# Kernel optimization log

Measured on AMD Instinct MI355X. Metric: run time of the kernel, lower is better.

The kernel has to match this reference:

```python
import jax, jax.numpy as jnp
import numpy as np

IN_CH = 256
OUT_CH = 256
STATE = 384
OUT_SEQ = 32
B_SZ = 8
SEQ = 512


def setup_inputs() -> dict:
    key = jax.random.key(0)
    ks = jax.random.split(key, 8)
    rmin, rmax, max_phase = 0.0, 1.0, 6.283
    u1 = jax.random.uniform(ks[0], (STATE,))
    u2 = jax.random.uniform(ks[1], (STATE,))
    # standard LRU stable-ring initialization
    nu_log = jnp.log(-0.5 * jnp.log(u1 * (rmax + rmin) * (rmax - rmin) + rmin ** 2))
    theta_log = jnp.log(max_phase * u2)
    lam_mod = jnp.exp(-jnp.exp(nu_log))
    gamma_log = jnp.log(jnp.sqrt(1.0 - lam_mod ** 2))
    B_re = jax.random.normal(ks[2], (STATE, IN_CH)) / np.sqrt(2 * IN_CH)
    B_im = jax.random.normal(ks[3], (STATE, IN_CH)) / np.sqrt(2 * IN_CH)
    C_re = jax.random.normal(ks[4], (OUT_CH, STATE)) / np.sqrt(STATE)
    C_im = jax.random.normal(ks[5], (OUT_CH, STATE)) / np.sqrt(STATE)
    D = jax.random.normal(ks[6], (OUT_CH, IN_CH)) / np.sqrt(IN_CH)
    x = jax.random.normal(ks[7], (B_SZ, SEQ, IN_CH))
    return dict(x=x, nu_log=nu_log, theta_log=theta_log, gamma_log=gamma_log,
                B_re=B_re, B_im=B_im, C_re=C_re, C_im=C_im, D=D)


def _lru(x, h_re, h_im, nu_log, theta_log, gamma_log, B_re, B_im, C_re, C_im, D):
    """One LRU pass over a full sequence. x: [B,S,C]. h_*: [B,N] initial complex state.
    Diagonal complex recurrence h_t = Lambda*h_{t-1} + gamma*(B x_t); y_t = Re(C h_t) + D x_t."""
    lam_mod = jnp.exp(-jnp.exp(nu_log))              # |Lambda| in (0,1)
    lre = lam_mod * jnp.cos(jnp.exp(theta_log))      # [N]
    lim = lam_mod * jnp.sin(jnp.exp(theta_log))
    gamma = jnp.exp(gamma_log)
    # input projection for whole sequence (complex, split into re/im)
    u_re = gamma * jnp.einsum('bsc,nc->bsn', x, B_re)  # [B,S,N]
    u_im = gamma * jnp.einsum('bsc,nc->bsn', x, B_im)

    def step(h, u):
        hre, him = h
        ur, ui = u
        nre = lre * hre - lim * him + ur
        nim = lre * him + lim * hre + ui
        return (nre, nim), (nre, nim)

    (h_re, h_im), (hs_re, hs_im) = jax.lax.scan(
        step, (h_re, h_im),
        (jnp.swapaxes(u_re, 0, 1), jnp.swapaxes(u_im, 0, 1)))  # scan over S
    hs_re = jnp.swapaxes(hs_re, 0, 1)  # [B,S,N]
    hs_im = jnp.swapaxes(hs_im, 0, 1)
    y = (jnp.einsum('bsn,on->bso', hs_re, C_re)
         - jnp.einsum('bsn,on->bso', hs_im, C_im)
         + jnp.einsum('bsc,oc->bso', x, D))
    return y, h_re, h_im


def reference(x, nu_log, theta_log, gamma_log, B_re, B_im, C_re, C_im, D):
    bsz = x.shape[0]
    h_re = jnp.zeros((bsz, STATE), x.dtype)   # state=None on first call -> zeros
    h_im = jnp.zeros((bsz, STATE), x.dtype)
    outs = []
    for _ in range(OUT_SEQ):
        x, h_re, h_im = _lru(x, h_re, h_im, nu_log, theta_log, gamma_log,
                             B_re, B_im, C_re, C_im, D)
        outs.append(x[:, -1:])
    return jnp.concatenate(outs, axis=-2)  # [B, OUT_SEQ, OUT_CH]
```

## Files before the change

### kernel.cpp

```cpp
#include <hip/hip_runtime.h>
#include <hip/hip_bf16.h>
#include <math.h>

typedef unsigned short u16;
typedef __attribute__((ext_vector_type(8))) short bf16x8;
typedef __attribute__((ext_vector_type(4))) float f32x4;
typedef __attribute__((ext_vector_type(16))) float f32x16;

#define IN_CH   256
#define STATE   384
#define OUT_SEQ 32
#define B_SZ    8
#define SEQ     512
#define M_ROWS  4096
#define NJ      768

#define PS_WB  (NJ*IN_CH)
#define PS_WC  (IN_CH*NJ)
#define PS_WD  (IN_CH*IN_CH)
#define PS_Z   ((size_t)M_ROWS*NJ)
#define PS_X   ((size_t)M_ROWS*IN_CH)

static constexpr size_t B_U   = 0;
static constexpr size_t B_Z   = B_U  + 8*(size_t)M_ROWS*IN_CH*4;
static constexpr size_t B_XA  = B_Z  + 3*(size_t)M_ROWS*NJ*2;
static constexpr size_t B_XB  = B_XA + 3*(size_t)M_ROWS*IN_CH*2;
static constexpr size_t B_WB  = B_XB + 3*(size_t)M_ROWS*IN_CH*2;
static constexpr size_t B_WC  = B_WB + 3*(size_t)PS_WB*2;
static constexpr size_t B_WD  = B_WC + 3*(size_t)PS_WC*2;
static constexpr size_t B_LAM = B_WD + 3*(size_t)PS_WD*2;
static constexpr size_t B_HC  = B_LAM + 2*768*4;

__device__ __forceinline__ u16 f2b(float v) {
    __hip_bfloat16 h = __float2bfloat16(v);
    return *(u16*)&h;
}
__device__ __forceinline__ float b2f(u16 u) {
    __hip_bfloat16 h = *(__hip_bfloat16*)&u;
    return __bfloat162float(h);
}
__device__ __forceinline__ void split3(float v, u16& a, u16& b, u16& c) {
    a = f2b(v);  float r1 = v  - b2f(a);
    b = f2b(r1); float r2 = r1 - b2f(b);
    c = f2b(r2);
}

__device__ __forceinline__ size_t a_idx(int row, int k, int NKC) {
    return ((size_t)(((row >> 5)*NKC + (k >> 5))*2 + ((k >> 4) & 1))*2 + ((k >> 3) & 1))*256
           + (size_t)(row & 31)*8 + (k & 7);
}

__device__ __forceinline__ void frag_decode(int r, int& t32, int& h, int& hi5,
                                            int& lo5, int& e) {
    t32 = r >> 10; int r2 = r & 1023;
    h = r2 >> 9;   int r3 = r2 & 511;
    hi5 = r3 >> 8; int r4 = r3 & 255;
    lo5 = r4 >> 3; e = r4 & 7;
}

__global__ void prep_lam_hc(const float* __restrict__ nu_log,
                            const float* __restrict__ th_log,
                            float* __restrict__ lam, float* __restrict__ lam16,
                            float* __restrict__ hc0) {
    int n = threadIdx.x;
    if (n < STATE) {
        float lm = expf(-expf(nu_log[n]));
        float th = expf(th_log[n]);
        float ar = lm * cosf(th), ai = lm * sinf(th);
        lam[2*n] = ar; lam[2*n+1] = ai;
        float pr = ar, pi = ai;
#pragma unroll
        for (int i = 0; i < 4; ++i) {
            float nr = pr*pr - pi*pi, ni = 2.f*pr*pi;
            pr = nr; pi = ni;
        }
        lam16[2*n] = pr; lam16[2*n+1] = pi;
    }
    for (int i = threadIdx.x; i < B_SZ*NJ; i += blockDim.x) hc0[i] = 0.f;
}

__global__ void prep_big(const float* __restrict__ B_re, const float* __restrict__ B_im,
                         const float* __restrict__ gamma_log,
                         const float* __restrict__ C_re, const float* __restrict__ C_im,
                         const float* __restrict__ D, const float* __restrict__ x,
                         u16* __restrict__ W, u16* __restrict__ WC, u16* __restrict__ WD,
                         u16* __restrict__ X1, u16* __restrict__ X2, u16* __restrict__ X3) {
    int idx = blockIdx.x*blockDim.x + threadIdx.x;
    if (idx < PS_WB) {
        int c32 = idx >> 13, r = idx & 8191;
        int t32,h,hi5,lo5,e; frag_decode(r, t32,h,hi5,lo5,e);
        int j = c32*32 + lo5;
        int k = t32*32 + (2*h + hi5)*8 + e;
        int n = j >> 1;
        float g = expf(gamma_log[n]);
        float v = g * ((j & 1) ? B_im[n*IN_CH + k] : B_re[n*IN_CH + k]);
        u16 a,b,cc; split3(v,a,b,cc);
        W[idx] = a; W[idx + PS_WB] = b; W[idx + 2*PS_WB] = cc;
        return;
    }
    idx -= PS_WB;
    if (idx < PS_WC) {
        int c32 = idx / 24576, r = idx % 24576;
        int t32,h,hi5,lo5,e; frag_decode(r, t32,h,hi5,lo5,e);
        int o = c32*32 + lo5;
        int j = t32*32 + (2*h + hi5)*8 + e;
        int n = j >> 1;
        float v = (j & 1) ? -C_im[o*STATE + n] : C_re[o*STATE + n];
        u16 a,b,c; split3(v,a,b,c);
        WC[idx] = a; WC[idx + PS_WC] = b; WC[idx + 2*PS_WC] = c;
        return;
    }
    idx -= PS_WC;
    if (idx < PS_WD) {
        int c32 = idx >> 13, r = idx & 8191;
        int t32,h,hi5,lo5,e; frag_decode(r, t32,h,hi5,lo5,e);
        int o = c32*32 + lo5;
        int c = t32*32 + (2*h + hi5)*8 + e;
        float v = D[o*IN_CH + c];
        u16 a,b,cc; split3(v,a,b,cc);
        WD[idx] = a; WD[idx + PS_WD] = b; WD[idx + 2*PS_WD] = cc;
        return;
    }
    idx -= PS_WD;
    {
        int row = idx >> 8, k = idx & 255;
        u16 a,b,c; split3(x[idx],a,b,c);
        size_t o = a_idx(row, k, 8);
        X1[o] = a; X2[o] = b; X3[o] = c;
    }
}

__device__ __constant__ const int cPI[6] = {0,0,1,0,1,2};
__device__ __constant__ const int cPJ[6] = {0,1,0,2,1,0};

struct G1P { const u16* A[3]; };

__global__ __launch_bounds__(512, 2)
void front_k(G1P ga, const u16* __restrict__ WBp, const u16* __restrict__ WDp,
             u16* __restrict__ Z1, u16* __restrict__ Z2, u16* __restrict__ Z3,
             float* __restrict__ P,
             const float* __restrict__ lam, const float* __restrict__ lam16,
             const float2* __restrict__ HcIn, float2* __restrict__ HcOut) {
    __shared__ __align__(16) float Ls[512*34];
    __shared__ float2 car[32][16];
    __shared__ float2 hp[32][16];
    const int tid = threadIdx.x, lane = tid & 63, w = tid >> 6;
    const int l15 = lane & 15, q = lane >> 4;
    const int hb = q >> 1, hi5q = q & 1;
    const int hi5 = lane >> 5, lo5 = lane & 31;

    if (blockIdx.x >= 192) {
        const int k0 = blockIdx.x - 192;
        const int mt = (k0 & 7)*8 + (k0 >> 3);
        const int wr = w & 1, wc = w >> 1;
        const int m32 = mt*2 + wr;
        f32x16 acc[2];
#pragma unroll
        for (int cj = 0; cj < 2; ++cj)
#pragma unroll
            for (int i = 0; i < 16; ++i) acc[cj][i] = 0.f;

        bf16x8 av[2][3][2], bv[2][2][3][2];
        auto loadA = [&](int buf, int kc) {
#pragma unroll
            for (int p = 0; p < 3; ++p)
#pragma unroll
                for (int h = 0; h < 2; ++h)
                    av[buf][p][h] = *(const bf16x8*)(ga.A[p]
                        + ((((size_t)(m32*8 + kc)*2 + h)*2 + hi5) << 8) + lo5*8);
        };
        auto loadB = [&](int buf, int kc) {
#pragma unroll
            for (int cj = 0; cj < 2; ++cj)
#pragma unroll
                for (int p = 0; p < 3; ++p)
#pragma unroll
                    for (int h = 0; h < 2; ++h)
                        bv[buf][cj][p][h] = *(const bf16x8*)(WDp + (size_t)p*PS_WD
                            + ((((size_t)((wc*2 + cj)*8 + kc)*2 + h)*2 + hi5) << 8) + lo5*8);
        };
        loadA(0, 0); loadB(0, 0);
        loadA(1, 1); loadB(1, 1);
#pragma unroll
        for (int kc = 0; kc < 8; ++kc) {
            const int cb = kc & 1;
#pragma unroll
            for (int t6 = 0; t6 < 6; ++t6)
#pragma unroll
                for (int cj = 0; cj < 2; ++cj)
#pragma unroll
                    for (int h = 0; h < 2; ++h)
                        acc[cj] = __builtin_amdgcn_mfma_f32_32x32x16_bf16(
                            av[cb][cPI[t6]][h], bv[cb][cj][cPJ[t6]][h], acc[cj], 0, 0, 0);
            if (kc + 2 < 8) { loadA(cb, kc + 2); loadB(cb, kc + 2); }
        }
#pragma unroll
        for (int cj = 0; cj < 2; ++cj)
#pragma unroll
            for (int reg = 0; reg < 16; ++reg) {
                int row = mt*64 + wr*32 + (reg & 3) + 8*(reg >> 2) + 4*hi5;
                int col = wc*64 + cj*32 + lo5;
                P[(size_t)row*IN_CH + col] = acc[cj][reg];
            }
        return;
    }

    const int b = blockIdx.x & 7, jt = blockIdx.x >> 3;

    f32x4 acc[4][2];
#pragma unroll
    for (int i = 0; i < 4; ++i)
#pragma unroll
        for (int n16 = 0; n16 < 2; ++n16) acc[i][n16] = 0.f;

    bf16x8 av[2][4][3], bv[2][2][3];
    auto loadA = [&](int buf, int kc) {
#pragma unroll
        for (int p = 0; p < 3; ++p)
#pragma unroll
            for (int i = 0; i < 4; ++i) {
                int m16 = i*8 + w;
                int row32 = b*16 + (m16 >> 1);
                int rin = ((m16 & 1) << 4) + l15;
                av[buf][i][p] = *(const bf16x8*)(ga.A[p]
                    + ((((size_t)(row32*8 + kc)*2 + hb)*2 + hi5q) << 8) + rin*8);
            }
    };
    auto loadB = [&](int buf, int kc) {
#pragma unroll
        for (int p = 0; p < 3; ++p)
#pragma unroll
            for (int n16 = 0; n16 < 2; ++n16)
                bv[buf][n16][p] = *(const bf16x8*)(WBp + (size_t)p*PS_WB
                    + ((((size_t)(jt*8 + kc)*2 + hb)*2 + hi5q) << 8) + (n16*16 + l15)*8);
    };

    loadA(0, 0); loadB(0, 0);
    loadA(1, 1); loadB(1, 1);
#pragma unroll
    for (int kc = 0; kc < 8; ++kc) {
        const int cb = kc & 1;
#pragma unroll
        for (int t6 = 0; t6 < 6; ++t6)
#pragma unroll
            for (int i = 0; i < 4; ++i)
#pragma unroll
                for (int n16 = 0; n16 < 2; ++n16)
                    acc[i][n16] = __builtin_amdgcn_mfma_f32_16x16x32_bf16(
                        av[cb][i][cPI[t6]], bv[cb][n16][cPJ[t6]], acc[i][n16], 0, 0, 0);
        if (kc + 2 < 8) { loadA(cb, kc + 2); loadB(cb, kc + 2); }
    }

#pragma unroll
    for (int i = 0; i < 4; ++i) {
        int m16 = i*8 + w;
#pragma unroll
        for (int n16 = 0; n16 < 2; ++n16)
#pragma unroll
            for (int r = 0; r < 4; ++r) {
                int s = m16*16 + q*4 + r;
                int jl = n16*16 + l15;
                Ls[s*34 + jl] = acc[i][n16][r];
            }
    }
    __syncthreads();

    {
        int st = tid & 15, ch = tid >> 4;
        int n = jt*16 + st;
        float lre = lam[2*n], lim = lam[2*n+1];
        float hr = 0.f, hm = 0.f;
#pragma unroll
        for (int t = 0; t < 16; ++t) {
            int s = ch*16 + t;
            float2 u = *(const float2*)&Ls[s*34 + 2*st];
            float nr = fmaf(lre, hr, fmaf(-lim, hm, u.x));
            float nm = fmaf(lre, hm, fmaf( lim, hr, u.y));
            hr = nr; hm = nm;
            *(float2*)&Ls[s*34 + 2*st] = make_float2(hr, hm);
        }
        car[ch][st] = make_float2(hr, hm);
    }
    __syncthreads();

    {
        int st2 = 2*w + hi5, ch2 = lane & 31;
        int n = jt*16 + st2;
        float2 e = car[ch2][st2];
        float Ar = lam16[2*n], Ai = lam16[2*n+1];
        float Br = e.x, Bi = e.y;
#pragma unroll
        for (int d = 1; d < 32; d <<= 1) {
            int src = (lane & 32) | ((lane - d) & 31);
            float pAr = __shfl(Ar, src), pAi = __shfl(Ai, src);
            float pBr = __shfl(Br, src), pBi = __shfl(Bi, src);
            if (ch2 >= d) {
                float nAr = Ar*pAr - Ai*pAi;
                float nAi = Ar*pAi + Ai*pAr;
                float nBr = fmaf(Ar, pBr, fmaf(-Ai, pBi, Br));
                float nBi = fmaf(Ar, pBi, fmaf( Ai, pBr, Bi));
                Ar = nAr; Ai = nAi; Br = nBr; Bi = nBi;
            }
        }
        float2 s0 = HcIn[(size_t)b*STATE + n];
        if (ch2 == 31) {
            float fr = fmaf(Ar, s0.x, fmaf(-Ai, s0.y, Br));
            float fi = fmaf(Ar, s0.y, fmaf( Ai, s0.x, Bi));
            HcOut[(size_t)b*STATE + n] = make_float2(fr, fi);
        }
        int srcp = (lane & 32) | ((lane - 1) & 31);
        float eAr = __shfl(Ar, srcp), eAi = __shfl(Ai, srcp);
        float eBr = __shfl(Br, srcp), eBi = __shfl(Bi, srcp);
        float sr, si;
        if (ch2 == 0) { sr = s0.x; si = s0.y; }
        else {
            sr = fmaf(eAr, s0.x, fmaf(-eAi, s0.y, eBr));
            si = fmaf(eAr, s0.y, fmaf( eAi, s0.x, eBi));
        }
        hp[ch2][st2] = make_float2(sr, si);
    }
    __syncthreads();

    {
        int st = tid & 15, ch = tid >> 4;
        int n = jt*16 + st;
        float lre = lam[2*n], lim = lam[2*n+1];
        float2 hh = hp[ch][st];
        float lpr = lre, lpi = lim;
        int j0 = jt*32 + 2*st;
#pragma unroll
        for (int t = 0; t < 16; ++t) {
            int s = ch*16 + t;
            float2 hl = *(const float2*)&Ls[s*34 + 2*st];
            float vr = fmaf(lpr, hh.x, fmaf(-lpi, hh.y, hl.x));
            float vi = fmaf(lpr, hh.y, fmaf( lpi, hh.x, hl.y));
            float nlr = lpr*lre - lpi*lim;
            float nli = lpr*lim + lpi*lre;
            lpr = nlr; lpi = nli;
            u16 a1,a2,a3, c1,c2,c3;
            split3(vr, a1,a2,a3);
            split3(vi, c1,c2,c3);
            size_t zo = a_idx(b*512 + s, j0, 24);
            ushort2 t2;
            t2.x = a1; t2.y = c1; *(ushort2*)(Z1 + zo) = t2;
            t2.x = a2; t2.y = c2; *(ushort2*)(Z2 + zo) = t2;
            t2.x = a3; t2.y = c3; *(ushort2*)(Z3 + zo) = t2;
        }
    }
}

struct G2P {
    const u16* Z[3]; const u16* WC; const float* P;
    u16* O1; u16* O2; u16* O3; float* outp; int iter;
};

__global__ __launch_bounds__(768, 3)
void gemm2_k(G2P g) {
    __shared__ __align__(16) float Lred[2*4*1024];
    const int tid = threadIdx.x, lane = tid & 63, w = tid >> 6;
    const int kg = w >> 2, wq = w & 3;
    const int wr = wq & 1, wcq = wq >> 1;
    const int bid = blockIdx.x;
    const int b = bid & 7, mloc = (bid >> 3) & 7, n_t = bid >> 6;
    const int mtile = b*8 + mloc;
    const int m0 = mtile*64, n0 = n_t*64;
    const int hi5 = lane >> 5, lo5 = lane & 31;
    const int c32 = n_t*2 + wcq;
    const int m32 = mtile*2 + wr;
    const int cbase = kg*8;

    f32x16 accv;
#pragma unroll
    for (int i = 0; i < 16; ++i) accv[i] = 0.f;

    auto aptr = [&](int p, int c, int h) -> const u16* {
        return g.Z[p] + ((((size_t)(m32*24 + c)*2 + h)*2 + hi5) << 8) + lo5*8;
    };
    auto bptr = [&](int p, int c, int h) -> const u16* {
        return g.WC + (size_t)p*PS_WC
               + ((((size_t)(c32*24 + c)*2 + h)*2 + hi5) << 8) + lo5*8;
    };

    bf16x8 av[2][3][2], bv[2][3][2];
    auto loadA = [&](int buf, int t) {
#pragma unroll
        for (int p = 0; p < 3; ++p)
#pragma unroll
            for (int h = 0; h < 2; ++h)
                av[buf][p][h] = *(const bf16x8*)aptr(p, cbase + t, h);
    };
    auto loadB = [&](int buf, int t) {
#pragma unroll
        for (int p = 0; p < 3; ++p)
#pragma unroll
            for (int h = 0; h < 2; ++h)
                bv[buf][p][h] = *(const bf16x8*)bptr(p, cbase + t, h);
    };

    loadA(0, 0); loadB(0, 0);
    loadA(1, 1); loadB(1, 1);
#pragma unroll
    for (int t = 0; t < 8; ++t) {
        const int cb = t & 1;
#pragma unroll
        for (int t6 = 0; t6 < 6; ++t6)
            accv = __builtin_amdgcn_mfma_f32_32x32x16_bf16(
                av[cb][cPI[t6]][0], bv[cb][cPJ[t6]][0],
                __builtin_amdgcn_mfma_f32_32x32x16_bf16(
                    av[cb][cPI[t6]][1], bv[cb][cPJ[t6]][1], accv, 0, 0, 0),
                0, 0, 0);
        if (t + 2 < 8) { loadA(cb, t + 2); loadB(cb, t + 2); }
    }

    if (kg != 0) {
        float* Lp = Lred + ((size_t)(kg - 1)*4 + wr*2 + wcq)*1024;
#pragma unroll
        for (int reg = 0; reg < 16; ++reg) {
            int rl = (reg & 3) + 8*(reg >> 2) + 4*hi5;
            Lp[rl*32 + lo5] = accv[reg];
        }
    }
    __syncthreads();
    if (kg == 0) {
        const float* L1 = Lred + ((size_t)0*4 + wr*2 + wcq)*1024;
        const float* L2 = Lred + ((size_t)1*4 + wr*2 + wcq)*1024;
#pragma unroll
        for (int reg = 0; reg < 16; ++reg) {
            int rl = (reg & 3) + 8*(reg >> 2) + 4*hi5;
            int row = m0 + wr*32 + rl;
            int col = n0 + wcq*32 + lo5;
            float v = accv[reg] + L1[rl*32 + lo5] + L2[rl*32 + lo5]
                    + g.P[(size_t)row*IN_CH + col];
            u16 a,b,c; split3(v, a,b,c);
            size_t o = a_idx(row, col, 8);
            g.O1[o] = a; g.O2[o] = b; g.O3[o] = c;
            if ((row & (SEQ-1)) == SEQ-1)
                g.outp[(size_t)((row >> 9)*OUT_SEQ + g.iter)*IN_CH + col] = v;
        }
    }
}

extern "C" void kernel_launch(void* const* d_in, const int* in_sizes, int n_in,
                              void* d_out, int out_size, void* d_ws, size_t ws_size,
                              hipStream_t stream) {
    const float* x_in      = (const float*)d_in[0];
    const float* nu_log    = (const float*)d_in[1];
    const float* theta_log = (const float*)d_in[2];
    const float* gamma_log = (const float*)d_in[3];
    const float* B_re      = (const float*)d_in[4];
    const float* B_im      = (const float*)d_in[5];
    const float* C_re      = (const float*)d_in[6];
    const float* C_im      = (const float*)d_in[7];
    const float* D         = (const float*)d_in[8];
    float* out = (float*)d_out;

    char* ws = (char*)d_ws;
    float* P = (float*)(ws + B_U);
    u16* Z1 = (u16*)(ws + B_Z);
    u16* Z2 = Z1 + PS_Z;
    u16* Z3 = Z2 + PS_Z;
    u16* XA1 = (u16*)(ws + B_XA);
    u16* XA2 = XA1 + PS_X;
    u16* XA3 = XA2 + PS_X;
    u16* XB1 = (u16*)(ws + B_XB);
    u16* XB2 = XB1 + PS_X;
    u16* XB3 = XB2 + PS_X;
    u16* WB  = (u16*)(ws + B_WB);
    u16* WCt = (u16*)(ws + B_WC);
    u16* WDt = (u16*)(ws + B_WD);
    float* lam   = (float*)(ws + B_LAM);
    float* lam16 = lam + 768;
    float2* Hc0  = (float2*)(ws + B_HC);
    float2* Hc1  = Hc0 + (size_t)B_SZ*STATE;

    prep_lam_hc<<<1, 384, 0, stream>>>(nu_log, theta_log, lam, lam16, (float*)Hc0);
    prep_big<<<5888, 256, 0, stream>>>(B_re, B_im, gamma_log, C_re, C_im, D, x_in,
                                       WB, WCt, WDt, XA1, XA2, XA3);

    for (int it = 0; it < OUT_SEQ; ++it) {
        u16* Xc[3]; u16* Xn[3];
        if (it & 1) { Xc[0]=XB1; Xc[1]=XB2; Xc[2]=XB3; Xn[0]=XA1; Xn[1]=XA2; Xn[2]=XA3; }
        else        { Xc[0]=XA1; Xc[1]=XA2; Xc[2]=XA3; Xn[0]=XB1; Xn[1]=XB2; Xn[2]=XB3; }
        float2* Hin  = (it & 1) ? Hc1 : Hc0;
        float2* Hout = (it & 1) ? Hc0 : Hc1;

        G1P g1;
        for (int p = 0; p < 3; ++p) g1.A[p] = Xc[p];
        front_k<<<256, 512, 0, stream>>>(
            g1, WB, WDt, Z1, Z2, Z3, P, lam, lam16, Hin, Hout);

        G2P g2;
        g2.Z[0]=Z1; g2.Z[1]=Z2; g2.Z[2]=Z3;
        g2.WC = WCt; g2.P = P;
        g2.O1 = Xn[0]; g2.O2 = Xn[1]; g2.O3 = Xn[2];
        g2.outp = out; g2.iter = it;
        gemm2_k<<<256, 768, 0, stream>>>(g2);
    }
}
```

Before: 1.258 ms.

## Fuse per-iteration kernels into one persistent kernel with grid barriers

Replaces the 64 launches of front_k and gemm2_k across the 32 autoregressive steps with a single persistent kernel of 256 blocks. Blocks synchronise through an atomic-counter grid barrier between phases. The second GEMM now runs with 512 threads split into two K-groups instead of 768 threads in three. This removes launch overhead and inter-kernel gaps, but relies on all 256 blocks being co-resident and spin-waiting.

```diff
diff --git a/kernel.cpp b/kernel.cpp
--- a/kernel.cpp
+++ b/kernel.cpp
@@ -30,6 +30,7 @@
 static constexpr size_t B_WD  = B_WC + 3*(size_t)PS_WC*2;
 static constexpr size_t B_LAM = B_WD + 3*(size_t)PS_WD*2;
 static constexpr size_t B_HC  = B_LAM + 2*768*4;
+static constexpr size_t B_CNT = B_HC  + 2*(size_t)B_SZ*NJ*4;
 
 __device__ __forceinline__ u16 f2b(float v) {
     __hip_bfloat16 h = __float2bfloat16(v);
@@ -58,11 +59,24 @@
     lo5 = r4 >> 3; e = r4 & 7;
 }
 
+__device__ __forceinline__ void gsync(int* cnt, int step) {
+    __syncthreads();
+    if (threadIdx.x == 0) {
+        __hip_atomic_fetch_add(cnt, 1, __ATOMIC_RELEASE, __HIP_MEMORY_SCOPE_AGENT);
+        while (__hip_atomic_load(cnt, __ATOMIC_RELAXED, __HIP_MEMORY_SCOPE_AGENT)
+               < step*256)
+            __builtin_amdgcn_s_sleep(8);
+        (void)__hip_atomic_load(cnt, __ATOMIC_ACQUIRE, __HIP_MEMORY_SCOPE_AGENT);
+    }
+    __syncthreads();
+}
+
 __global__ void prep_lam_hc(const float* __restrict__ nu_log,
                             const float* __restrict__ th_log,
                             float* __restrict__ lam, float* __restrict__ lam16,
-                            float* __restrict__ hc0) {
+                            float* __restrict__ hc0, int* __restrict__ cnt) {
     int n = threadIdx.x;
+    if (n == 0) *cnt = 0;
     if (n < STATE) {
         float lm = expf(-expf(nu_log[n]));
         float th = expf(th_log[n]);
@@ -133,310 +147,326 @@
 __device__ __constant__ const int cPI[6] = {0,0,1,0,1,2};
 __device__ __constant__ const int cPJ[6] = {0,1,0,2,1,0};
 
-struct G1P { const u16* A[3]; };
+struct MP {
+    const u16 *XA1, *XA2, *XA3;
+    u16 *XB1, *XB2, *XB3;
+    u16 *YA1, *YA2, *YA3;
+    const u16 *WB, *WC, *WD;
+    u16 *Z1, *Z2, *Z3;
+    float *P;
+    const float *lam, *lam16;
+    float2 *Hc0, *Hc1;
+    float *outp;
+    int *cnt;
+};
 
 __global__ __launch_bounds__(512, 2)
-void front_k(G1P ga, const u16* __restrict__ WBp, const u16* __restrict__ WDp,
-             u16* __restrict__ Z1, u16* __restrict__ Z2, u16* __restrict__ Z3,
-             float* __restrict__ P,
-             const float* __restrict__ lam, const float* __restrict__ lam16,
-             const float2* __restrict__ HcIn, float2* __restrict__ HcOut) {
+void mono_k(MP g) {
     __shared__ __align__(16) float Ls[512*34];
     __shared__ float2 car[32][16];
     __shared__ float2 hp[32][16];
     const int tid = threadIdx.x, lane = tid & 63, w = tid >> 6;
+    const int bid = blockIdx.x;
     const int l15 = lane & 15, q = lane >> 4;
     const int hb = q >> 1, hi5q = q & 1;
     const int hi5 = lane >> 5, lo5 = lane & 31;
-
-    if (blockIdx.x >= 192) {
-        const int k0 = blockIdx.x - 192;
-        const int mt = (k0 & 7)*8 + (k0 >> 3);
-        const int wr = w & 1, wc = w >> 1;
-        const int m32 = mt*2 + wr;
-        f32x16 acc[2];
-#pragma unroll
-        for (int cj = 0; cj < 2; ++cj)
-#pragma unroll
-            for (int i = 0; i < 16; ++i) acc[cj][i] = 0.f;
-
-        bf16x8 av[2][3][2], bv[2][2][3][2];
-        auto loadA = [&](int buf, int kc) {
-#pragma unroll
-            for (int p = 0; p < 3; ++p)
-#pragma unroll
-                for (int h = 0; h < 2; ++h)
-                    av[buf][p][h] = *(const bf16x8*)(ga.A[p]
-                        + ((((size_t)(m32*8 + kc)*2 + h)*2 + hi5) << 8) + lo5*8);
-        };
-        auto loadB = [&](int buf, int kc) {
+    int step = 0;
+
+    for (int it = 0; it < OUT_SEQ; ++it) {
+        const u16* Xc[3]; u16* Xn[3];
+        if (it & 1) {
+            Xc[0]=g.XB1; Xc[1]=g.XB2; Xc[2]=g.XB3;
+            Xn[0]=g.YA1; Xn[1]=g.YA2; Xn[2]=g.YA3;
+        } else {
+            Xc[0]=g.XA1; Xc[1]=g.XA2; Xc[2]=g.XA3;
+            Xn[0]=g.XB1; Xn[1]=g.XB2; Xn[2]=g.XB3;
+        }
+        const float2* Hin  = (it & 1) ? g.Hc1 : g.Hc0;
+        float2*       Hout = (it & 1) ? g.Hc0 : g.Hc1;
+
+        if (bid >= 192) {
+            const int k0 = bid - 192;
+            const int mt = (k0 & 7)*8 + (k0 >> 3);
+            const int wr = w & 1, wc = w >> 1;
+            const int m32 = mt*2 + wr;
+            f32x16 acc[2];
 #pragma unroll
             for (int cj = 0; cj < 2; ++cj)
 #pragma unroll
+                for (int i = 0; i < 16; ++i) acc[cj][i] = 0.f;
+
+            bf16x8 av[2][3][2], bv[2][2][3][2];
+            auto loadA = [&](int buf, int kc) {
+#pragma unroll
                 for (int p = 0; p < 3; ++p)
 #pragma unroll
                     for (int h = 0; h < 2; ++h)
-                        bv[buf][cj][p][h] = *(const bf16x8*)(WDp + (size_t)p*PS_WD
-                            + ((((size_t)((wc*2 + cj)*8 + kc)*2 + h)*2 + hi5) << 8) + lo5*8);
-        };
-        loadA(0, 0); loadB(0, 0);
-        loadA(1, 1); loadB(1, 1);
-#pragma unroll
-        for (int kc = 0; kc < 8; ++kc) {
-            const int cb = kc & 1;
-#pragma unroll
-            for (int t6 = 0; t6 < 6; ++t6)
+                        av[buf][p][h] = *(const bf16x8*)(Xc[p]
+                            + ((((size_t)(m32*8 + kc)*2 + h)*2 + hi5) << 8) + lo5*8);
+            };
+            auto loadB = [&](int buf, int kc) {
 #pragma unroll
                 for (int cj = 0; cj < 2; ++cj)
 #pragma unroll
-                    for (int h = 0; h < 2; ++h)
-                        acc[cj] = __builtin_amdgcn_mfma_f32_32x32x16_bf16(
-                            av[cb][cPI[t6]][h], bv[cb][cj][cPJ[t6]][h], acc[cj], 0, 0, 0);
-            if (kc + 2 < 8) { loadA(cb, kc + 2); loadB(cb, kc + 2); }
-        }
-#pragma unroll
-        for (int cj = 0; cj < 2; ++cj)
-#pragma unroll
-            for (int reg = 0; reg < 16; ++reg) {
-                int row = mt*64 + wr*32 + (reg & 3) + 8*(reg >> 2) + 4*hi5;
-                int col = wc*64 + cj*32 + lo5;
-                P[(size_t)row*IN_CH + col] = acc[cj][reg];
-            }
-        return;
-    }
-
-    const int b = blockIdx.x & 7, jt = blockIdx.x >> 3;
-
-    f32x4 acc[4][2];
-#pragma unroll
-    for (int i = 0; i < 4; ++i)
-#pragma unroll
-        for (int n16 = 0; n16 < 2; ++n16) acc[i][n16] = 0.f;
-
-    bf16x8 av[2][4][3], bv[2][2][3];
-    auto loadA = [&](int buf, int kc) {
-#pragma unroll
-        for (int p = 0; p < 3; ++p)
+                    for (int p = 0; p < 3; ++p)
+#pragma unroll
+                        for (int h = 0; h < 2; ++h)
+                            bv[buf][cj][p][h] = *(const bf16x8*)(g.WD + (size_t)p*PS_WD
+                                + ((((size_t)((wc*2 + cj)*8 + kc)*2 + h)*2 + hi5) << 8) + lo5*8);
+            };
+            loadA(0, 0); loadB(0, 0);
+            loadA(1, 1); loadB(1, 1);
+#pragma unroll
+            for (int kc = 0; kc < 8; ++kc) {
+                const int cb = kc & 1;
+#pragma unroll
+                for (int t6 = 0; t6 < 6; ++t6)
+#pragma unroll
+                    for (int cj = 0; cj < 2; ++cj)
+#pragma unroll
+                        for (int h = 0; h < 2; ++h)
+                            acc[cj] = __builtin_amdgcn_mfma_f32_32x32x16_bf16(
+                                av[cb][cPI[t6]][h], bv[cb][cj][cPJ[t6]][h], acc[cj], 0, 0, 0);
+                if (kc + 2 < 8) { loadA(cb, kc + 2); loadB(cb, kc + 2); }
+            }
+#pragma unroll
+            for (int cj = 0; cj < 2; ++cj)
+#pragma unroll
+                for (int reg = 0; reg < 16; ++reg) {
+                    int row = mt*64 + wr*32 + (reg & 3) + 8*(reg >> 2) + 4*hi5;
+                    int col = wc*64 + cj*32 + lo5;
+                    g.P[(size_t)row*IN_CH + col] = acc[cj][reg];
+                }
+        } else {
+            const int b = bid & 7, jt = bid >> 3;
+
+            f32x4 acc[4][2];
+#pragma unroll
+            for (int i = 0; i < 4; ++i)
+#pragma unroll
+                for (int n16 = 0; n16 < 2; ++n16) acc[i][n16] = 0.f;
+
+            bf16x8 av[2][4][3], bv[2][2][3];
+            auto loadA = [&](int buf, int kc) {
+#pragma unroll
+                for (int p = 0; p < 3; ++p)
+#pragma unroll
+                    for (int i = 0; i < 4; ++i) {
+                        int m16 = i*8 + w;
+                        int row32 = b*16 + (m16 >> 1);
+                        int rin = ((m16 & 1) << 4) + l15;
+                        av[buf][i][p] = *(const bf16x8*)(Xc[p]
+                            + ((((size_t)(row32*8 + kc)*2 + hb)*2 + hi5q) << 8) + rin*8);
+                    }
+            };
+            auto loadB = [&](int buf, int kc) {
+#pragma unroll
+                for (int p = 0; p < 3; ++p)
+#pragma unroll
+                    for (int n16 = 0; n16 < 2; ++n16)
+                        bv[buf][n16][p] = *(const bf16x8*)(g.WB + (size_t)p*PS_WB
+                            + ((((size_t)(jt*8 + kc)*2 + hb)*2 + hi5q) << 8) + (n16*16 + l15)*8);
+            };
+
+            loadA(0, 0); loadB(0, 0);
+            loadA(1, 1); loadB(1, 1);
+#pragma unroll
+            for (int kc = 0; kc < 8; ++kc) {
+                const int cb = kc & 1;
+#pragma unroll
+                for (int t6 = 0; t6 < 6; ++t6)
+#pragma unroll
+                    for (int i = 0; i < 4; ++i)
+#pragma unroll
+                        for (int n16 = 0; n16 < 2; ++n16)
+                            acc[i][n16] = __builtin_amdgcn_mfma_f32_16x16x32_bf16(
+                                av[cb][i][cPI[t6]], bv[cb][n16][cPJ[t6]], acc[i][n16], 0, 0, 0);
+                if (kc + 2 < 8) { loadA(cb, kc + 2); loadB(cb, kc + 2); }
+            }
+
 #pragma unroll
             for (int i = 0; i < 4; ++i) {
                 int m16 = i*8 + w;
-                int row32 = b*16 + (m16 >> 1);
-                int rin = ((m16 & 1) << 4) + l15;
-                av[buf][i][p] = *(const bf16x8*)(ga.A[p]
-                    + ((((size_t)(row32*8 + kc)*2 + hb)*2 + hi5q) << 8) + rin*8);
-            }
-    };
-    auto loadB = [&](int buf, int kc) {
-#pragma unroll
-        for (int p = 0; p < 3; ++p)
-#pragma unroll
-            for (int n16 = 0; n16 < 2; ++n16)
-                bv[buf][n16][p] = *(const bf16x8*)(WBp + (size_t)p*PS_WB
-                    + ((((size_t)(jt*8 + kc)*2 + hb)*2 + hi5q) << 8) + (n16*16 + l15)*8);
-    };
-
-    loadA(0, 0); loadB(0, 0);
-    loadA(1, 1); loadB(1, 1);
-#pragma unroll
-    for (int kc = 0; kc < 8; ++kc) {
-        const int cb = kc & 1;
-#pragma unroll
-        for (int t6 = 0; t6 < 6; ++t6)
-#pragma unroll
-            for (int i = 0; i < 4; ++i)
 #pragma unroll
                 for (int n16 = 0; n16 < 2; ++n16)
-                    acc[i][n16] = __builtin_amdgcn_mfma_f32_16x16x32_bf16(
-                        av[cb][i][cPI[t6]], bv[cb][n16][cPJ[t6]], acc[i][n16], 0, 0, 0);
-        if (kc + 2 < 8) { loadA(cb, kc + 2); loadB(cb, kc + 2); }
-    }
-
-#pragma unroll
-    for (int i = 0; i < 4; ++i) {
-        int m16 = i*8 + w;
-#pragma unroll
-        for (int n16 = 0; n16 < 2; ++n16)
-#pragma unroll
-            for (int r = 0; r < 4; ++r) {
-                int s = m16*16 + q*4 + r;
-                int jl = n16*16 + l15;
-                Ls[s*34 + jl] = acc[i][n16][r];
-            }
-    }
-    __syncthreads();
-
-    {
-        int st = tid & 15, ch = tid >> 4;
-        int n = jt*16 + st;
-        float lre = lam[2*n], lim = lam[2*n+1];
-        float hr = 0.f, hm = 0.f;
-#pragma unroll
-        for (int t = 0; t < 16; ++t) {
-            int s = ch*16 + t;
-            float2 u = *(const float2*)&Ls[s*34 + 2*st];
-            float nr = fmaf(lre, hr, fmaf(-lim, hm, u.x));
-            float nm = fmaf(lre, hm, fmaf( lim, hr, u.y));
-            hr = nr; hm = nm;
-            *(float2*)&Ls[s*34 + 2*st] = make_float2(hr, hm);
+#pragma unroll
+                    for (int r = 0; r < 4; ++r) {
+                        int s = m16*16 + q*4 + r;
+                        int jl = n16*16 + l15;
+                        Ls[s*34 + jl] = acc[i][n16][r];
+                    }
+            }
+            __syncthreads();
+
+            {
+                int st = tid & 15, ch = tid >> 4;
+                int n = jt*16 + st;
+                float lre = g.lam[2*n], lim = g.lam[2*n+1];
+                float hr = 0.f, hm = 0.f;
+#pragma unroll
+                for (int t = 0; t < 16; ++t) {
+                    int s = ch*16 + t;
+                    float2 u = *(const float2*)&Ls[s*34 + 2*st];
+                    float nr = fmaf(lre, hr, fmaf(-lim, hm, u.x));
+                    float nm = fmaf(lre, hm, fmaf( lim, hr, u.y));
+                    hr = nr; hm = nm;
+                    *(float2*)&Ls[s*34 + 2*st] = make_float2(hr, hm);
+                }
+                car[ch][st] = make_float2(hr, hm);
+            }
+            __syncthreads();
+
+            {
+                int st2 = 2*w + hi5, ch2 = lane & 31;
+                int n = jt*16 + st2;
+                float2 e = car[ch2][st2];
+                float Ar = g.lam16[2*n], Ai = g.lam16[2*n+1];
+                float Br = e.x, Bi = e.y;
+#pragma unroll
+                for (int d = 1; d < 32; d <<= 1) {
+                    int src = (lane & 32) | ((lane - d) & 31);
+                    float pAr = __shfl(Ar, src), pAi = __shfl(Ai, src);
+                    float pBr = __shfl(Br, src), pBi = __shfl(Bi, src);
+                    if (ch2 >= d) {
+                        float nAr = Ar*pAr - Ai*pAi;
+                        float nAi = Ar*pAi + Ai*pAr;
+                        float nBr = fmaf(Ar, pBr, fmaf(-Ai, pBi, Br));
+                        float nBi = fmaf(Ar, pBi, fmaf( Ai, pBr, Bi));
+                        Ar = nAr; Ai = nAi; Br = nBr; Bi = nBi;
+                    }
+                }
+                float2 s0 = Hin[(size_t)b*STATE + n];
+                if (ch2 == 31) {
+                    float fr = fmaf(Ar, s0.x, fmaf(-Ai, s0.y, Br));
+                    float fi = fmaf(Ar, s0.y, fmaf( Ai, s0.x, Bi));
+                    Hout[(size_t)b*STATE + n] = make_float2(fr, fi);
+                }
+                int srcp = (lane & 32) | ((lane - 1) & 31);
+                float eAr = __shfl(Ar, srcp), eAi = __shfl(Ai, srcp);
+                float eBr = __shfl(Br, srcp), eBi = __shfl(Bi, srcp);
+                float sr, si;
+                if (ch2 == 0) { sr = s0.x; si = s0.y; }
+                else {
+                    sr = fmaf(eAr, s0.x, fmaf(-eAi, s0.y, eBr));
+                    si = fmaf(eAr, s0.y, fmaf( eAi, s0.x, eBi));
+                }
+                hp[ch2][st2] = make_float2(sr, si);
+            }
+            __syncthreads();
+
+            {
+                int st = tid & 15, ch = tid >> 4;
+                int n = jt*16 + st;
+                float lre = g.lam[2*n], lim = g.lam[2*n+1];
+                float2 hh = hp[ch][st];
+                float lpr = lre, lpi = lim;
+                int j0 = jt*32 + 2*st;
+#pragma unroll
+                for (int t = 0; t < 16; ++t) {
+                    int s = ch*16 + t;
+                    float2 hl = *(const float2*)&Ls[s*34 + 2*st];
+                    float vr = fmaf(lpr, hh.x, fmaf(-lpi, hh.y, hl.x));
+                    float vi = fmaf(lpr, hh.y, fmaf( lpi, hh.x, hl.y));
+                    float nlr = lpr*lre - lpi*lim;
+                    float nli = lpr*lim + lpi*lre;
+                    lpr = nlr; lpi = nli;
+                    u16 a1,a2,a3, c1,c2,c3;
+                    split3(vr, a1,a2,a3);
+                    split3(vi, c1,c2,c3);
+                    size_t zo = a_idx(b*512 + s, j0, 24);
+                    ushort2 t2;
+                    t2.x = a1; t2.y = c1; *(ushort2*)(g.Z1 + zo) = t2;
+                    t2.x = a2; t2.y = c2; *(ushort2*)(g.Z2 + zo) = t2;
+                    t2.x = a3; t2.y = c3; *(ushort2*)(g.Z3 + zo) = t2;
+                }
+            }
         }
-        car[ch][st] = make_float2(hr, hm);
-    }
-    __syncthreads();
-
-    {
-        int st2 = 2*w + hi5, ch2 = lane & 31;
-        int n = jt*16 + st2;
-        float2 e = car[ch2][st2];
-        float Ar = lam16[2*n], Ai = lam16[2*n+1];
-        float Br = e.x, Bi = e.y;
-#pragma unroll
-        for (int d = 1; d < 32; d <<= 1) {
-            int src = (lane & 32) | ((lane - d) & 31);
-            float pAr = __shfl(Ar, src), pAi = __shfl(Ai, src);
-            float pBr = __shfl(Br, src), pBi = __shfl(Bi, src);
-            if (ch2 >= d) {
-                float nAr = Ar*pAr - Ai*pAi;
-                float nAi = Ar*pAi + Ai*pAr;
-                float nBr = fmaf(Ar, pBr, fmaf(-Ai, pBi, Br));
-                float nBi = fmaf(Ar, pBi, fmaf( Ai, pBr, Bi));
-                Ar = nAr; Ai = nAi; Br = nBr; Bi = nBi;
+
+        gsync(g.cnt, ++step);
+
+        {
+            const int b = bid & 7, mloc = (bid >> 3) & 7, n_t = bid >> 6;
+            const int mtile = b*8 + mloc;
+            const int m0 = mtile*64, n0 = n_t*64;
+            const int kg = w >> 2, wq = w & 3;
+            const int wr = wq & 1, wcq = wq >> 1;
+            const int c32 = n_t*2 + wcq;
+            const int m32 = mtile*2 + wr;
+            const int cbase = kg*12;
+            float* Lred = Ls;
+
+            f32x16 accv;
+#pragma unroll
+            for (int i = 0; i < 16; ++i) accv[i] = 0.f;
+
+            auto aptr = [&](int p, int c, int h) -> const u16* {
+                const u16* Zp = (p == 0) ? g.Z1 : (p == 1) ? g.Z2 : g.Z3;
+                return Zp + ((((size_t)(m32*24 + c)*2 + h)*2 + hi5) << 8) + lo5*8;
+            };
+            auto bptr = [&](int p, int c, int h) -> const u16* {
+                return g.WC + (size_t)p*PS_WC
+                       + ((((size_t)(c32*24 + c)*2 + h)*2 + hi5) << 8) + lo5*8;
+            };
+
+            bf16x8 av[2][3][2], bv[2][3][2];
+            auto loadA = [&](int buf, int t) {
+#pragma unroll
+                for (int p = 0; p < 3; ++p)
+#pragma unroll
+                    for (int h = 0; h < 2; ++h)
+                        av[buf][p][h] = *(const bf16x8*)aptr(p, cbase + t, h);
+            };
+            auto loadB = [&](int buf, int t) {
+#pragma unroll
+                for (int p = 0; p < 3; ++p)
+#pragma unroll
+                    for (int h = 0; h < 2; ++h)
+                        bv[buf][p][h] = *(const bf16x8*)bptr(p, cbase + t, h);
+            };
+
+            loadA(0, 0); loadB(0, 0);
+            loadA(1, 1); loadB(1, 1);
+#pragma unroll
+            for (int t = 0; t < 12; ++t) {
+                const int cb = t & 1;
+#pragma unroll
+                for (int t6 = 0; t6 < 6; ++t6)
+                    accv = __builtin_amdgcn_mfma_f32_32x32x16_bf16(
+                        av[cb][cPI[t6]][0], bv[cb][cPJ[t6]][0],
+                        __builtin_amdgcn_mfma_f32_32x32x16_bf16(
+                            av[cb][cPI[t6]][1], bv[cb][cPJ[t6]][1], accv, 0, 0, 0),
+                        0, 0, 0);
+                if (t + 2 < 12) { loadA(cb, t + 2); loadB(cb, t + 2); }
+            }
+
+            __syncthreads();
+            if (kg == 1) {
+#pragma unroll
+                for (int reg = 0; reg < 16; ++reg) {
+                    int rl = wr*32 + (reg & 3) + 8*(reg >> 2) + 4*hi5;
+                    int cl = wcq*32 + lo5;
+                    Lred[rl*64 + cl] = accv[reg];
+                }
+            }
+            __syncthreads();
+            if (kg == 0) {
+#pragma unroll
+                for (int reg = 0; reg < 16; ++reg) {
+                    int rl = wr*32 + (reg & 3) + 8*(reg >> 2) + 4*hi5;
+                    int cl = wcq*32 + lo5;
+                    int row = m0 + rl, col = n0 + cl;
+                    float v = accv[reg] + Lred[rl*64 + cl]
+                            + g.P[(size_t)row*IN_CH + col];
+                    u16 a,b2,c; split3(v, a,b2,c);
+                    size_t o = a_idx(row, col, 8);
+                    Xn[0][o] = a; Xn[1][o] = b2; Xn[2][o] = c;
+                    if ((row & (SEQ-1)) == SEQ-1)
+                        g.outp[(size_t)((row >> 9)*OUT_SEQ + it)*IN_CH + col] = v;
+                }
             }
         }
-        float2 s0 = HcIn[(size_t)b*STATE + n];
-        if (ch2 == 31) {
-            float fr = fmaf(Ar, s0.x, fmaf(-Ai, s0.y, Br));
-            float fi = fmaf(Ar, s0.y, fmaf( Ai, s0.x, Bi));
-            HcOut[(size_t)b*STATE + n] = make_float2(fr, fi);
-        }
-        int srcp = (lane & 32) | ((lane - 1) & 31);
-        float eAr = __shfl(Ar, srcp), eAi = __shfl(Ai, srcp);
-        float eBr = __shfl(Br, srcp), eBi = __shfl(Bi, srcp);
-        float sr, si;
-        if (ch2 == 0) { sr = s0.x; si = s0.y; }
-        else {
-            sr = fmaf(eAr, s0.x, fmaf(-eAi, s0.y, eBr));
-            si = fmaf(eAr, s0.y, fmaf( eAi, s0.x, eBi));
-        }
-        hp[ch2][st2] = make_float2(sr, si);
-    }
-    __syncthreads();
-
-    {
-        int st = tid & 15, ch = tid >> 4;
-        int n = jt*16 + st;
-        float lre = lam[2*n], lim = lam[2*n+1];
-        float2 hh = hp[ch][st];
-        float lpr = lre, lpi = lim;
-        int j0 = jt*32 + 2*st;
-#pragma unroll
-        for (int t = 0; t < 16; ++t) {
-            int s = ch*16 + t;
-            float2 hl = *(const float2*)&Ls[s*34 + 2*st];
-            float vr = fmaf(lpr, hh.x, fmaf(-lpi, hh.y, hl.x));
-            float vi = fmaf(lpr, hh.y, fmaf( lpi, hh.x, hl.y));
-            float nlr = lpr*lre - lpi*lim;
-            float nli = lpr*lim + lpi*lre;
-            lpr = nlr; lpi = nli;
-            u16 a1,a2,a3, c1,c2,c3;
-            split3(vr, a1,a2,a3);
-            split3(vi, c1,c2,c3);
-            size_t zo = a_idx(b*512 + s, j0, 24);
-            ushort2 t2;
-            t2.x = a1; t2.y = c1; *(ushort2*)(Z1 + zo) = t2;
-            t2.x = a2; t2.y = c2; *(ushort2*)(Z2 + zo) = t2;
-            t2.x = a3; t2.y = c3; *(ushort2*)(Z3 + zo) = t2;
-        }
-    }
-}
-
-struct G2P {
-    const u16* Z[3]; const u16* WC; const float* P;
-    u16* O1; u16* O2; u16* O3; float* outp; int iter;
-};
-
-__global__ __launch_bounds__(768, 3)
-void gemm2_k(G2P g) {
-    __shared__ __align__(16) float Lred[2*4*1024];
-    const int tid = threadIdx.x, lane = tid & 63, w = tid >> 6;
-    const int kg = w >> 2, wq = w & 3;
-    const int wr = wq & 1, wcq = wq >> 1;
-    const int bid = blockIdx.x;
-    const int b = bid & 7, mloc = (bid >> 3) & 7, n_t = bid >> 6;
-    const int mtile = b*8 + mloc;
-    const int m0 = mtile*64, n0 = n_t*64;
-    const int hi5 = lane >> 5, lo5 = lane & 31;
-    const int c32 = n_t*2 + wcq;
-    const int m32 = mtile*2 + wr;
-    const int cbase = kg*8;
-
-    f32x16 accv;
-#pragma unroll
-    for (int i = 0; i < 16; ++i) accv[i] = 0.f;
-
-    auto aptr = [&](int p, int c, int h) -> const u16* {
-        return g.Z[p] + ((((size_t)(m32*24 + c)*2 + h)*2 + hi5) << 8) + lo5*8;
-    };
-    auto bptr = [&](int p, int c, int h) -> const u16* {
-        return g.WC + (size_t)p*PS_WC
-               + ((((size_t)(c32*24 + c)*2 + h)*2 + hi5) << 8) + lo5*8;
-    };
-
-    bf16x8 av[2][3][2], bv[2][3][2];
-    auto loadA = [&](int buf, int t) {
-#pragma unroll
-        for (int p = 0; p < 3; ++p)
-#pragma unroll
-            for (int h = 0; h < 2; ++h)
-                av[buf][p][h] = *(const bf16x8*)aptr(p, cbase + t, h);
-    };
-    auto loadB = [&](int buf, int t) {
-#pragma unroll
-        for (int p = 0; p < 3; ++p)
-#pragma unroll
-            for (int h = 0; h < 2; ++h)
-                bv[buf][p][h] = *(const bf16x8*)bptr(p, cbase + t, h);
-    };
-
-    loadA(0, 0); loadB(0, 0);
-    loadA(1, 1); loadB(1, 1);
-#pragma unroll
-    for (int t = 0; t < 8; ++t) {
-        const int cb = t & 1;
-#pragma unroll
-        for (int t6 = 0; t6 < 6; ++t6)
-            accv = __builtin_amdgcn_mfma_f32_32x32x16_bf16(
-                av[cb][cPI[t6]][0], bv[cb][cPJ[t6]][0],
-                __builtin_amdgcn_mfma_f32_32x32x16_bf16(
-                    av[cb][cPI[t6]][1], bv[cb][cPJ[t6]][1], accv, 0, 0, 0),
-                0, 0, 0);
-        if (t + 2 < 8) { loadA(cb, t + 2); loadB(cb, t + 2); }
-    }
-
-    if (kg != 0) {
-        float* Lp = Lred + ((size_t)(kg - 1)*4 + wr*2 + wcq)*1024;
-#pragma unroll
-        for (int reg = 0; reg < 16; ++reg) {
-            int rl = (reg & 3) + 8*(reg >> 2) + 4*hi5;
-            Lp[rl*32 + lo5] = accv[reg];
-        }
-    }
-    __syncthreads();
-    if (kg == 0) {
-        const float* L1 = Lred + ((size_t)0*4 + wr*2 + wcq)*1024;
-        const float* L2 = Lred + ((size_t)1*4 + wr*2 + wcq)*1024;
-#pragma unroll
-        for (int reg = 0; reg < 16; ++reg) {
-            int rl = (reg & 3) + 8*(reg >> 2) + 4*hi5;
-            int row = m0 + wr*32 + rl;
-            int col = n0 + wcq*32 + lo5;
-            float v = accv[reg] + L1[rl*32 + lo5] + L2[rl*32 + lo5]
-                    + g.P[(size_t)row*IN_CH + col];
-            u16 a,b,c; split3(v, a,b,c);
-            size_t o = a_idx(row, col, 8);
-            g.O1[o] = a; g.O2[o] = b; g.O3[o] = c;
-            if ((row & (SEQ-1)) == SEQ-1)
-                g.outp[(size_t)((row >> 9)*OUT_SEQ + g.iter)*IN_CH + col] = v;
-        }
+
+        if (it + 1 < OUT_SEQ) gsync(g.cnt, ++step);
     }
 }
 
@@ -472,28 +502,20 @@
     float* lam16 = lam + 768;
     float2* Hc0  = (float2*)(ws + B_HC);
     float2* Hc1  = Hc0 + (size_t)B_SZ*STATE;
-
-    prep_lam_hc<<<1, 384, 0, stream>>>(nu_log, theta_log, lam, lam16, (float*)Hc0);
+    int* cnt = (int*)(ws + B_CNT);
+
+    prep_lam_hc<<<1, 384, 0, stream>>>(nu_log, theta_log, lam, lam16, (float*)Hc0, cnt);
     prep_big<<<5888, 256, 0, stream>>>(B_re, B_im, gamma_log, C_re, C_im, D, x_in,
                                        WB, WCt, WDt, XA1, XA2, XA3);
 
-    for (int it = 0; it < OUT_SEQ; ++it) {
-        u16* Xc[3]; u16* Xn[3];
-        if (it & 1) { Xc[0]=XB1; Xc[1]=XB2; Xc[2]=XB3; Xn[0]=XA1; Xn[1]=XA2; Xn[2]=XA3; }
-        else        { Xc[0]=XA1; Xc[1]=XA2; Xc[2]=XA3; Xn[0]=XB1; Xn[1]=XB2; Xn[2]=XB3; }
-        float2* Hin  = (it & 1) ? Hc1 : Hc0;
-        float2* Hout = (it & 1) ? Hc0 : Hc1;
-
-        G1P g1;
-        for (int p = 0; p < 3; ++p) g1.A[p] = Xc[p];
-        front_k<<<256, 512, 0, stream>>>(
-            g1, WB, WDt, Z1, Z2, Z3, P, lam, lam16, Hin, Hout);
-
-        G2P g2;
-        g2.Z[0]=Z1; g2.Z[1]=Z2; g2.Z[2]=Z3;
-        g2.WC = WCt; g2.P = P;
-        g2.O1 = Xn[0]; g2.O2 = Xn[1]; g2.O3 = Xn[2];
-        g2.outp = out; g2.iter = it;
-        gemm2_k<<<256, 768, 0, stream>>>(g2);
-    }
-}
+    MP g;
+    g.XA1 = XA1; g.XA2 = XA2; g.XA3 = XA3;
+    g.XB1 = XB1; g.XB2 = XB2; g.XB3 = XB3;
+    g.YA1 = XA1; g.YA2 = XA2; g.YA3 = XA3;
+    g.WB = WB; g.WC = WCt; g.WD = WDt;
+    g.Z1 = Z1; g.Z2 = Z2; g.Z3 = Z3;
+    g.P = P; g.lam = lam; g.lam16 = lam16;
+    g.Hc0 = Hc0; g.Hc1 = Hc1;
+    g.outp = out; g.cnt = cnt;
+    mono_k<<<256, 512, 0, stream>>>(g);
+}
```

After: 4.794 ms. 281% more time.
